# Kernel tuning notes

Hardware: AMD Instinct MI355X
Metric: run time of the kernel (lower is better)

## Reference

```python
import jax, jax.numpy as jnp
import numpy as np

B, C_IN, C_MID, C_OUT, R, K = 2048, 64, 64, 128, 60, 13
EPS = 1e-5


def _gather(x, nei):
    # x: [B, C, 60] -> gather neighbors -> [B, C, 60, 13]
    b, c = x.shape[0], x.shape[1]
    return x[:, :, nei].reshape(b, c, R, K)


def _block(x, nei, g, bta, m, v, W, c):
    # BN (eval mode) -> ReLU -> Conv2d(kernel (1,13)) fused block.
    h = _gather(x, nei)                              # [B,C,60,13]
    inv = g * jax.lax.rsqrt(v + EPS)                 # [C]
    h = jax.nn.relu(h * inv[None, :, None, None] + (bta - m * inv)[None, :, None, None])
    # Conv2d with kernel (1,13), stride 1 == contraction over (c, k)
    return jnp.einsum('bcrk,ock->bor', h, W) + c[None, :, None]  # [B,O,60]


def setup_inputs() -> dict:
    key = jax.random.key(0)
    ks = jax.random.split(key, 24)
    n = lambda k, s: jax.random.normal(k, s, dtype=jnp.float32)
    u = lambda k, s: jax.random.uniform(k, s, dtype=jnp.float32, minval=0.5, maxval=1.5)
    return {
        "x": n(ks[0], (B, C_IN, R)),
        "nei": jax.random.randint(ks[1], (R * K,), 0, R, dtype=jnp.int32),
        # comb_layer_in: BN(in) + Conv(in->mid)
        "g1": n(ks[2], (C_IN,)), "b1": n(ks[3], (C_IN,)), "m1": n(ks[4], (C_IN,)), "v1": u(ks[5], (C_IN,)),
        "W1": n(ks[6], (C_MID, C_IN, K)) * 0.1, "c1": n(ks[7], (C_MID,)) * 0.1,
        # comb_layer_out: BN(mid) + Conv(mid->out)
        "g2": n(ks[8], (C_MID,)), "b2": n(ks[9], (C_MID,)), "m2": n(ks[10], (C_MID,)), "v2": u(ks[11], (C_MID,)),
        "W2": n(ks[12], (C_OUT, C_MID, K)) * 0.1, "c2": n(ks[13], (C_OUT,)) * 0.1,
        # short_cut_layer: BN(in) + Conv(in->out)
        "g3": n(ks[14], (C_IN,)), "b3": n(ks[15], (C_IN,)), "m3": n(ks[16], (C_IN,)), "v3": u(ks[17], (C_IN,)),
        "W3": n(ks[18], (C_OUT, C_IN, K)) * 0.1, "c3": n(ks[19], (C_OUT,)) * 0.1,
    }


def reference(x, nei, g1, b1, m1, v1, W1, c1, g2, b2, m2, v2, W2, c2,
              g3, b3, m3, v3, W3, c3):
    f = _block(x, nei, g1, b1, m1, v1, W1, c1)      # [B, C_MID, 60]
    f = _block(f, nei, g2, b2, m2, v2, W2, c2)      # [B, C_OUT, 60]
    sc = _block(x, nei, g3, b3, m3, v3, W3, c3)     # [B, C_OUT, 60]
    return f + sc
```

## Files before the change

### kernel.cpp

```cpp
#include <hip/hip_runtime.h>
#include <hip/hip_bf16.h>


typedef __attribute__((ext_vector_type(8))) short bf16x8;
typedef __attribute__((ext_vector_type(4))) float f32x4;
typedef __attribute__((ext_vector_type(4))) unsigned short us4;
typedef __attribute__((ext_vector_type(8))) unsigned short us8;

#define EPSV 1e-5f
#define PLANE 131072
#define ZTOT  7864320

__device__ __forceinline__ unsigned short f2bf(float f) {
  unsigned int u = __builtin_bit_cast(unsigned int, f);
  u += 0x7FFFu + ((u >> 16) & 1u);
  return (unsigned short)(u >> 16);
}
__device__ __forceinline__ float bf2f(unsigned short s) {
  unsigned int u = ((unsigned int)s) << 16;
  return __builtin_bit_cast(float, u);
}

typedef const __attribute__((address_space(1))) unsigned int gas_u32;
typedef __attribute__((address_space(3))) unsigned int las_u32;
__device__ __forceinline__ void gl16(const void* g, void* l) {
  __builtin_amdgcn_global_load_lds((gas_u32*)g, (las_u32*)l, 16, 0, 0);
}

__global__ void prep_w(const float* __restrict__ W1, const float* __restrict__ W2,
                       const float* __restrict__ W3,
                       const float* __restrict__ g1, const float* __restrict__ be1,
                       const float* __restrict__ mu1, const float* __restrict__ va1,
                       const float* __restrict__ c1,
                       const float* __restrict__ g2, const float* __restrict__ be2,
                       const float* __restrict__ mu2, const float* __restrict__ va2,
                       const float* __restrict__ c2,
                       const float* __restrict__ g3, const float* __restrict__ be3,
                       const float* __restrict__ mu3, const float* __restrict__ va3,
                       const float* __restrict__ c3,
                       unsigned short* __restrict__ W1t,
                       unsigned short* __restrict__ W23t,
                       float* __restrict__ params) {
  int t = blockIdx.x * 256 + threadIdx.x;
  if (t < 4096) {
    int o = t >> 6, c = t & 63;
    const float* src = W1 + (o * 64 + c) * 13;
    unsigned short* dst = W1t + o * 832 + c;
    #pragma unroll
    for (int ks = 0; ks < 13; ks++) dst[ks * 64] = f2bf(src[ks]);
  } else if (t < 20480) {
    int idx = t - 4096;
    int half = idx >> 13;
    int o = (idx >> 6) & 127, c = idx & 63;
    const float* src = (half ? W3 : W2) + (o * 64 + c) * 13;
    unsigned short* dst = W23t + o * 1664 + half * 13 * 64 + c;
    #pragma unroll
    for (int ks = 0; ks < 13; ks++) dst[ks * 64] = f2bf(src[ks]);
  }
  if (blockIdx.x == 79) {
    int u = threadIdx.x;
    if (u < 64) {
      float a1v = g1[u] * rsqrtf(va1[u] + EPSV);
      params[u]       = a1v;
      params[64 + u]  = be1[u] - mu1[u] * a1v;
      float a3v = g3[u] * rsqrtf(va3[u] + EPSV);
      params[128 + u] = a3v;
      params[192 + u] = be3[u] - mu3[u] * a3v;
      float a2v = g2[u] * rsqrtf(va2[u] + EPSV);
      params[256 + u] = a2v;
      params[320 + u] = be2[u] - mu2[u] * a2v + a2v * c1[u];
    }
    if (u < 128) params[384 + u] = c2[u] + c3[u];
  }
}

__global__ __launch_bounds__(256) void t_in(const float* __restrict__ x,
                                            const float* __restrict__ params,
                                            unsigned short* __restrict__ z1T,
                                            unsigned short* __restrict__ z3T) {
  __shared__ float xt[64 * 61];
  __shared__ float prm[256];
  const int b = blockIdx.x, t = threadIdx.x;
  prm[t] = params[t];
  for (int i = t; i < 3840; i += 256) {
    int c = i / 60;
    xt[c * 61 + (i - c * 60)] = x[b * 3840 + i];
  }
  __syncthreads();
  if (t < 240) {
    int r = t >> 2, g = t & 3, c0 = g << 4;
    us8 z1v0, z1v1, z3v0, z3v1;
    #pragma unroll
    for (int j = 0; j < 8; j++) {
      int c = c0 + j;
      float v = xt[c * 61 + r];
      z1v0[j] = f2bf(fmaxf(fmaf(v, prm[c], prm[64 + c]), 0.f));
      z3v0[j] = f2bf(fmaxf(fmaf(v, prm[128 + c], prm[192 + c]), 0.f));
    }
    #pragma unroll
    for (int j = 0; j < 8; j++) {
      int c = c0 + 8 + j;
      float v = xt[c * 61 + r];
      z1v1[j] = f2bf(fmaxf(fmaf(v, prm[c], prm[64 + c]), 0.f));
      z3v1[j] = f2bf(fmaxf(fmaf(v, prm[128 + c], prm[192 + c]), 0.f));
    }
    int idx = (r * 2048 + b) * 64 + c0;
    *(us8*)(z1T + idx) = z1v0;  *(us8*)(z1T + idx + 8) = z1v1;
    *(us8*)(z3T + idx) = z3v0;  *(us8*)(z3T + idx + 8) = z3v1;
  }
}

#define MFMA __builtin_amdgcn_mfma_f32_16x16x32_bf16

__global__ __launch_bounds__(256, 2) void gemm1(const unsigned short* __restrict__ W1t,
                                                const unsigned short* __restrict__ z1T,
                                                const int* __restrict__ nei,
                                                const float* __restrict__ params,
                                                unsigned short* __restrict__ z2T) {
  __shared__ unsigned short As[2][4096];
  __shared__ unsigned short Bs[2][2][8192];

  const int bid = blockIdx.x;
  const int rp = bid >> 4, btile = bid & 15;
  const int b0 = btile << 7;
  const int rA = rp * 2, rB = rA + 1;
  const int t = threadIdx.x, wave = t >> 6, lane = t & 63;
  const int quad = lane >> 4, nl = lane & 15;
  const int rsel = wave >> 1, nhh = wave & 1;

  int pl0[13], pl1[13];
  #pragma unroll
  for (int q = 0; q < 13; q++) { pl0[q] = nei[rA * 13 + q]; pl1[q] = nei[rB * 13 + q]; }

  const int trow = t >> 3, tj = t & 7;
  const int sw8 = ((tj ^ (trow & 7)) << 3);
  const unsigned short* gA = W1t + trow * 832 + tj * 8;
  const unsigned short* gB = z1T + (b0 + trow) * 64 + tj * 8;
  unsigned short* lA = &As[0][trow * 64 + sw8];
  unsigned short* lB0 = &Bs[0][0][trow * 64 + sw8];
  unsigned short* lB1 = &Bs[0][1][trow * 64 + sw8];

  {
    us8 va0 = *(const us8*)(gA);
    us8 va1 = *(const us8*)(gA + 32 * 832);
    const unsigned short* g0 = gB + pl0[0] * PLANE;
    const unsigned short* g1p = gB + pl1[0] * PLANE;
    us8 b00 = *(const us8*)(g0);
    us8 b01 = *(const us8*)(g0 + 2048);
    us8 b02 = *(const us8*)(g0 + 4096);
    us8 b03 = *(const us8*)(g0 + 6144);
    us8 b10 = *(const us8*)(g1p);
    us8 b11 = *(const us8*)(g1p + 2048);
    us8 b12 = *(const us8*)(g1p + 4096);
    us8 b13 = *(const us8*)(g1p + 6144);
    *(us8*)(lA) = va0;  *(us8*)(lA + 2048) = va1;
    *(us8*)(lB0) = b00; *(us8*)(lB0 + 2048) = b01;
    *(us8*)(lB0 + 4096) = b02; *(us8*)(lB0 + 6144) = b03;
    *(us8*)(lB1) = b10; *(us8*)(lB1 + 2048) = b11;
    *(us8*)(lB1 + 4096) = b12; *(us8*)(lB1 + 6144) = b13;
  }
  __syncthreads();

  const int c0 = ((quad ^ (nl & 7)) << 3);
  f32x4 acc[4][4] = {};
  #pragma unroll 1
  for (int kq = 0; kq < 13; kq++) {
    const int bf = kq & 1;
    us8 va0, va1, b00, b01, b02, b03, b10, b11, b12, b13;
    if (kq < 12) {
      const unsigned short* ga = gA + (kq + 1) * 64;
      va0 = *(const us8*)(ga);
      va1 = *(const us8*)(ga + 32 * 832);
      const unsigned short* g0 = gB + pl0[kq + 1] * PLANE;
      const unsigned short* g1p = gB + pl1[kq + 1] * PLANE;
      b00 = *(const us8*)(g0);        b01 = *(const us8*)(g0 + 2048);
      b02 = *(const us8*)(g0 + 4096); b03 = *(const us8*)(g0 + 6144);
      b10 = *(const us8*)(g1p);        b11 = *(const us8*)(g1p + 2048);
      b12 = *(const us8*)(g1p + 4096); b13 = *(const us8*)(g1p + 6144);
    }
    const unsigned short* Ab = &As[bf][nl * 64];
    const unsigned short* Bb = &Bs[bf][rsel][(nhh * 64 + nl) * 64];
    bf16x8 af[4][2], bfr[4][2];
    #pragma unroll
    for (int mt = 0; mt < 4; mt++) {
      af[mt][0] = *(const bf16x8*)(Ab + mt * 1024 + c0);
      af[mt][1] = *(const bf16x8*)(Ab + mt * 1024 + (c0 ^ 32));
    }
    #pragma unroll
    for (int nt = 0; nt < 4; nt++) {
      bfr[nt][0] = *(const bf16x8*)(Bb + nt * 1024 + c0);
      bfr[nt][1] = *(const bf16x8*)(Bb + nt * 1024 + (c0 ^ 32));
    }
    #pragma unroll
    for (int h = 0; h < 2; h++)
      #pragma unroll
      for (int mt = 0; mt < 4; mt++)
        #pragma unroll
        for (int nt = 0; nt < 4; nt++)
          acc[mt][nt] = MFMA(af[mt][h], bfr[nt][h], acc[mt][nt], 0, 0, 0);
    if (kq < 12) {
      unsigned short* la = lA + (bf ^ 1) * 4096;
      unsigned short* l0 = lB0 + (bf ^ 1) * 16384;
      unsigned short* l1 = lB1 + (bf ^ 1) * 16384;
      *(us8*)(la) = va0;  *(us8*)(la + 2048) = va1;
      *(us8*)(l0) = b00; *(us8*)(l0 + 2048) = b01;
      *(us8*)(l0 + 4096) = b02; *(us8*)(l0 + 6144) = b03;
      *(us8*)(l1) = b10; *(us8*)(l1 + 2048) = b11;
      *(us8*)(l1 + 4096) = b12; *(us8*)(l1 + 6144) = b13;
    }
    __syncthreads();
  }

  const int rr = rA + rsel;
  #pragma unroll
  for (int mt = 0; mt < 4; mt++) {
    int ob = mt * 16 + quad * 4;
    f32x4 av = *(const f32x4*)(params + 256 + ob);
    f32x4 bv = *(const f32x4*)(params + 320 + ob);
    #pragma unroll
    for (int nt = 0; nt < 4; nt++) {
      int col = b0 + nhh * 64 + nt * 16 + nl;
      f32x4 a = acc[mt][nt];
      us4 w;
      w.x = f2bf(fmaxf(fmaf(a[0], av[0], bv[0]), 0.f));
      w.y = f2bf(fmaxf(fmaf(a[1], av[1], bv[1]), 0.f));
      w.z = f2bf(fmaxf(fmaf(a[2], av[2], bv[2]), 0.f));
      w.w = f2bf(fmaxf(fmaf(a[3], av[3], bv[3]), 0.f));
      *(us4*)(z2T + (rr * 2048 + col) * 64 + ob) = w;
    }
  }
}

__global__ __launch_bounds__(256, 1) void gemm2(const unsigned short* __restrict__ W23t,
                                                const unsigned short* __restrict__ z2T,
                                                const unsigned short* __restrict__ z3T,
                                                const int* __restrict__ nei,
                                                const float* __restrict__ params,
                                                unsigned short* __restrict__ outT) {
  __shared__ unsigned short As[2][8192];
  __shared__ unsigned short Bs[2][16384];

  const int bid = blockIdx.x;
  const int r = bid >> 3, btile = bid & 7;
  const int b0 = btile << 8;
  const int t = threadIdx.x, wv = t >> 6, lane = t & 63;
  const int quad = lane >> 4, nl = lane & 15;
  const int mh = wv >> 1, nh = wv & 1;

  const int lr = lane >> 3, lj = lane & 7;
  const int swz = ((lj ^ lr) << 4);
  int aoff[4];
  #pragma unroll
  for (int i = 0; i < 4; i++) aoff[i] = (wv * 32 + i * 8 + lr) * 3328 + swz;
  int boff[8];
  #pragma unroll
  for (int i = 0; i < 8; i++) boff[i] = (b0 + wv * 64 + i * 8 + lr) * 128 + swz;

  const char* gAb = (const char*)W23t;
  const int neibase = r * 13;

  {
    int p0 = nei[neibase];
    const char* gb = (const char*)(z2T + p0 * PLANE);
    #pragma unroll
    for (int i = 0; i < 4; i++)
      gl16(gAb + aoff[i], &As[0][(4 * wv + i) * 512]);
    #pragma unroll
    for (int i = 0; i < 8; i++)
      gl16(gb + boff[i], &Bs[0][(8 * wv + i) * 512]);
  }
  asm volatile("s_waitcnt vmcnt(0)" ::: "memory");
  __syncthreads();

  const int c0 = ((quad ^ (nl & 7)) << 3);
  f32x4 acc[4][8] = {};
  #pragma unroll 1
  for (int kq = 0; kq < 26; kq++) {
    const int buf = kq & 1;
    if (kq < 25) {
      const int kn = kq + 1;
      int p = nei[neibase + (kn < 13 ? kn : kn - 13)];
      const char* ga = gAb + kn * 128;
      const char* gb = (const char*)((kn < 13 ? z2T : z3T) + p * PLANE);
      #pragma unroll
      for (int i = 0; i < 4; i++)
        gl16(ga + aoff[i], &As[buf ^ 1][(4 * wv + i) * 512]);
      #pragma unroll
      for (int i = 0; i < 8; i++)
        gl16(gb + boff[i], &Bs[buf ^ 1][(8 * wv + i) * 512]);
    }
    const unsigned short* Ab = &As[buf][(mh * 64 + nl) * 64];
    const unsigned short* Bb = &Bs[buf][(nh * 128 + nl) * 64];
    #pragma unroll
    for (int h = 0; h < 2; h++) {
      const int cc = h ? (c0 ^ 32) : c0;
      bf16x8 af[4], bfr[8];
      #pragma unroll
      for (int mt = 0; mt < 4; mt++)
        af[mt] = *(const bf16x8*)(Ab + mt * 1024 + cc);
      #pragma unroll
      for (int nt = 0; nt < 8; nt++)
        bfr[nt] = *(const bf16x8*)(Bb + nt * 1024 + cc);
      #pragma unroll
      for (int mt = 0; mt < 4; mt++)
        #pragma unroll
        for (int nt = 0; nt < 8; nt++)
          acc[mt][nt] = MFMA(af[mt], bfr[nt], acc[mt][nt], 0, 0, 0);
    }
    asm volatile("s_waitcnt vmcnt(0)" ::: "memory");
    __syncthreads();
  }

  #pragma unroll
  for (int mt = 0; mt < 4; mt++) {
    int ob = mh * 64 + mt * 16 + quad * 4;
    f32x4 cv = *(const f32x4*)(params + 384 + ob);
    #pragma unroll
    for (int nt = 0; nt < 8; nt++) {
      int col = b0 + nh * 128 + nt * 16 + nl;
      f32x4 a = acc[mt][nt];
      us4 w;
      w.x = f2bf(a[0] + cv[0]);
      w.y = f2bf(a[1] + cv[1]);
      w.z = f2bf(a[2] + cv[2]);
      w.w = f2bf(a[3] + cv[3]);
      *(us4*)(outT + (r * 2048 + col) * 128 + ob) = w;
    }
  }
}

__global__ __launch_bounds__(256) void t_out(const unsigned short* __restrict__ outT,
                                             float* __restrict__ out) {
  __shared__ float ot[60 * 129];
  const int b = blockIdx.x, t = threadIdx.x;
  for (int i = t; i < 1920; i += 256) {
    int r = i >> 5, og = (i & 31) << 2;
    us4 v = *(const us4*)(outT + (r * 2048 + b) * 128 + og);
    ot[r * 129 + og + 0] = bf2f(v.x);
    ot[r * 129 + og + 1] = bf2f(v.y);
    ot[r * 129 + og + 2] = bf2f(v.z);
    ot[r * 129 + og + 3] = bf2f(v.w);
  }
  __syncthreads();
  int o = t >> 1, s = t & 1;
  float* dst = out + b * 7680 + o * 60 + s * 30;
  #pragma unroll
  for (int j = 0; j < 30; j++) dst[j] = ot[(s * 30 + j) * 129 + o];
}

extern "C" void kernel_launch(void* const* d_in, const int* in_sizes, int n_in,
                              void* d_out, int out_size, void* d_ws, size_t ws_size,
                              hipStream_t stream) {
  const float* x   = (const float*)d_in[0];
  const int*   nei = (const int*)d_in[1];
  const float* g1  = (const float*)d_in[2];
  const float* be1 = (const float*)d_in[3];
  const float* mu1 = (const float*)d_in[4];
  const float* va1 = (const float*)d_in[5];
  const float* W1  = (const float*)d_in[6];
  const float* c1  = (const float*)d_in[7];
  const float* g2  = (const float*)d_in[8];
  const float* be2 = (const float*)d_in[9];
  const float* mu2 = (const float*)d_in[10];
  const float* va2 = (const float*)d_in[11];
  const float* W2  = (const float*)d_in[12];
  const float* c2  = (const float*)d_in[13];
  const float* g3  = (const float*)d_in[14];
  const float* be3 = (const float*)d_in[15];
  const float* mu3 = (const float*)d_in[16];
  const float* va3 = (const float*)d_in[17];
  const float* W3  = (const float*)d_in[18];
  const float* c3  = (const float*)d_in[19];

  unsigned short* W1t  = (unsigned short*)d_ws;
  unsigned short* W23t = W1t + 53248;
  float*          prm  = (float*)(W23t + 212992);
  unsigned short* z2T  = (unsigned short*)(prm + 512);
  unsigned short* z3T  = z2T + ZTOT;
  unsigned short* big  = z3T + ZTOT;
  unsigned short* z1T  = big;
  unsigned short* outT = big;

  prep_w<<<80, 256, 0, stream>>>(W1, W2, W3,
                                 g1, be1, mu1, va1, c1,
                                 g2, be2, mu2, va2, c2,
                                 g3, be3, mu3, va3, c3,
                                 W1t, W23t, prm);
  t_in<<<2048, 256, 0, stream>>>(x, prm, z1T, z3T);
  gemm1<<<480, 256, 0, stream>>>(W1t, z1T, nei, prm, z2T);
  gemm2<<<480, 256, 0, stream>>>(W23t, z2T, z3T, nei, prm, outT);
  t_out<<<2048, 256, 0, stream>>>(outT, (float*)d_out);
}
```

Before: 265.8 us.

## Halve gemm2 K-step to 32 channels and allow two blocks per CU

Splits each 64-channel K-step of gemm2 into two 32-channel half-steps, so each LDS double buffer holds half as much data. With the smaller shared-memory footprint the launch bounds now request two blocks per CU, aiming to raise occupancy and hide global-load latency. The cost is twice as many loop iterations and barriers, and the XOR swizzle is dropped, which may bring back LDS bank conflicts. The register cap implied by two blocks could also force spills of the 128-float accumulator.

```diff
diff --git a/kernel.cpp b/kernel.cpp
--- a/kernel.cpp
+++ b/kernel.cpp
@@ -231,14 +231,14 @@
   }
 }
 
-__global__ __launch_bounds__(256, 1) void gemm2(const unsigned short* __restrict__ W23t,
+__global__ __launch_bounds__(256, 2) void gemm2(const unsigned short* __restrict__ W23t,
                                                 const unsigned short* __restrict__ z2T,
                                                 const unsigned short* __restrict__ z3T,
                                                 const int* __restrict__ nei,
                                                 const float* __restrict__ params,
                                                 unsigned short* __restrict__ outT) {
-  __shared__ unsigned short As[2][8192];
-  __shared__ unsigned short Bs[2][16384];
+  __shared__ unsigned short As[2][4096];
+  __shared__ unsigned short Bs[2][8192];
 
   const int bid = blockIdx.x;
   const int r = bid >> 3, btile = bid & 7;
@@ -247,66 +247,62 @@
   const int quad = lane >> 4, nl = lane & 15;
   const int mh = wv >> 1, nh = wv & 1;
 
-  const int lr = lane >> 3, lj = lane & 7;
-  const int swz = ((lj ^ lr) << 4);
-  int aoff[4];
-  #pragma unroll
-  for (int i = 0; i < 4; i++) aoff[i] = (wv * 32 + i * 8 + lr) * 3328 + swz;
-  int boff[8];
-  #pragma unroll
-  for (int i = 0; i < 8; i++) boff[i] = (b0 + wv * 64 + i * 8 + lr) * 128 + swz;
+  const int neibase = r * 13;
+
+  const int lr = lane >> 2, lj = lane & 3;
+  int aoff[2];
+  #pragma unroll
+  for (int i = 0; i < 2; i++) aoff[i] = (16 * (2 * wv + i) + lr) * 3328 + lj * 16;
+  int boff[4];
+  #pragma unroll
+  for (int i = 0; i < 4; i++) boff[i] = (b0 + 16 * (4 * wv + i) + lr) * 128 + lj * 16;
 
   const char* gAb = (const char*)W23t;
-  const int neibase = r * 13;
 
   {
     int p0 = nei[neibase];
     const char* gb = (const char*)(z2T + p0 * PLANE);
     #pragma unroll
+    for (int i = 0; i < 2; i++)
+      gl16(gAb + aoff[i], &As[0][(2 * wv + i) * 512]);
+    #pragma unroll
     for (int i = 0; i < 4; i++)
-      gl16(gAb + aoff[i], &As[0][(4 * wv + i) * 512]);
-    #pragma unroll
-    for (int i = 0; i < 8; i++)
-      gl16(gb + boff[i], &Bs[0][(8 * wv + i) * 512]);
+      gl16(gb + boff[i], &Bs[0][(4 * wv + i) * 512]);
   }
   asm volatile("s_waitcnt vmcnt(0)" ::: "memory");
   __syncthreads();
 
-  const int c0 = ((quad ^ (nl & 7)) << 3);
   f32x4 acc[4][8] = {};
   #pragma unroll 1
-  for (int kq = 0; kq < 26; kq++) {
-    const int buf = kq & 1;
-    if (kq < 25) {
-      const int kn = kq + 1;
-      int p = nei[neibase + (kn < 13 ? kn : kn - 13)];
-      const char* ga = gAb + kn * 128;
-      const char* gb = (const char*)((kn < 13 ? z2T : z3T) + p * PLANE);
+  for (int s = 0; s < 52; s++) {
+    const int buf = s & 1;
+    if (s < 51) {
+      const int kn = s + 1;
+      const int pn = kn >> 1, hn = kn & 1;
+      int p = nei[neibase + (pn < 13 ? pn : pn - 13)];
+      const char* ga = gAb + pn * 128 + hn * 64;
+      const char* gb = (const char*)((pn < 13 ? z2T : z3T) + p * PLANE) + hn * 64;
+      #pragma unroll
+      for (int i = 0; i < 2; i++)
+        gl16(ga + aoff[i], &As[buf ^ 1][(2 * wv + i) * 512]);
       #pragma unroll
       for (int i = 0; i < 4; i++)
-        gl16(ga + aoff[i], &As[buf ^ 1][(4 * wv + i) * 512]);
-      #pragma unroll
-      for (int i = 0; i < 8; i++)
-        gl16(gb + boff[i], &Bs[buf ^ 1][(8 * wv + i) * 512]);
-    }
-    const unsigned short* Ab = &As[buf][(mh * 64 + nl) * 64];
-    const unsigned short* Bb = &Bs[buf][(nh * 128 + nl) * 64];
-    #pragma unroll
-    for (int h = 0; h < 2; h++) {
-      const int cc = h ? (c0 ^ 32) : c0;
-      bf16x8 af[4], bfr[8];
-      #pragma unroll
-      for (int mt = 0; mt < 4; mt++)
-        af[mt] = *(const bf16x8*)(Ab + mt * 1024 + cc);
+        gl16(gb + boff[i], &Bs[buf ^ 1][(4 * wv + i) * 512]);
+    }
+    const unsigned short* Ab = &As[buf][(mh * 64 + nl) * 32 + quad * 8];
+    const unsigned short* Bb = &Bs[buf][(nh * 128 + nl) * 32 + quad * 8];
+    bf16x8 af[4], bfr[8];
+    #pragma unroll
+    for (int mt = 0; mt < 4; mt++)
+      af[mt] = *(const bf16x8*)(Ab + mt * 512);
+    #pragma unroll
+    for (int nt = 0; nt < 8; nt++)
+      bfr[nt] = *(const bf16x8*)(Bb + nt * 512);
+    #pragma unroll
+    for (int mt = 0; mt < 4; mt++)
       #pragma unroll
       for (int nt = 0; nt < 8; nt++)
-        bfr[nt] = *(const bf16x8*)(Bb + nt * 1024 + cc);
-      #pragma unroll
-      for (int mt = 0; mt < 4; mt++)
-        #pragma unroll
-        for (int nt = 0; nt < 8; nt++)
-          acc[mt][nt] = MFMA(af[mt], bfr[nt], acc[mt][nt], 0, 0, 0);
-    }
+        acc[mt][nt] = MFMA(af[mt], bfr[nt], acc[mt][nt], 0, 0, 0);
     asm volatile("s_waitcnt vmcnt(0)" ::: "memory");
     __syncthreads();
   }
```

New measurement: 245.0 us. -7.8%, faster.
